# Kernel tuning notes

Hardware: AMD Instinct MI355X
Metric: run time of the kernel (lower is better)

## Reference

```python
import jax, jax.numpy as jnp
import numpy as np

DIM = 1024
NUM_HEADS = 16
HEAD_DIM = DIM // NUM_HEADS
SCALE = HEAD_DIM ** (-0.5)


def setup_inputs() -> dict:
    key = jax.random.key(0)
    ks = jax.random.split(key, 5)
    B, L, D = 2, 2048, DIM
    x = jax.random.normal(ks[0], (B, L, D), dtype=jnp.float32)
    # torch nn.Linear init scale ~ U(-1/sqrt(fan_in), 1/sqrt(fan_in)); use small normals
    s = 1.0 / np.sqrt(D)
    qkv_w = jax.random.uniform(ks[1], (3 * D, D), minval=-s, maxval=s, dtype=jnp.float32)
    qkv_b = jax.random.uniform(ks[2], (3 * D,), minval=-s, maxval=s, dtype=jnp.float32)
    proj_w = jax.random.uniform(ks[3], (D, D), minval=-s, maxval=s, dtype=jnp.float32)
    proj_b = jax.random.uniform(ks[4], (D,), minval=-s, maxval=s, dtype=jnp.float32)
    return {"x": x, "qkv_w": qkv_w, "qkv_b": qkv_b, "proj_w": proj_w, "proj_b": proj_b}


def reference(x, qkv_w, qkv_b, proj_w, proj_b):
    B, L, D = x.shape
    H, Hd = NUM_HEADS, HEAD_DIM
    # QKV projection: [B,L,3D] -> [3,B,H,L,Hd]
    qkv = x @ qkv_w.T + qkv_b
    qkv = qkv.reshape(B, L, 3, H, Hd).transpose(2, 0, 3, 1, 4)
    q, k, v = qkv[0], qkv[1], qkv[2]
    scores = jnp.einsum('bhqd,bhkd->bhqk', q, k) * SCALE  # [B,H,L,L]
    attn = jax.nn.softmax(scores, axis=-1)
    out = jnp.einsum('bhqk,bhkd->bhqd', attn, v)  # [B,H,L,Hd]
    out = out.transpose(0, 2, 1, 3).reshape(B, L, D)
    out = out @ proj_w.T + proj_b
    return out
```

## Files before the change

kernel.cpp:

```cpp
#include <hip/hip_runtime.h>
#include <hip/hip_bf16.h>
#include <cstdint>
#include <cstddef>

#define D_MODEL 1024
#define NHEADS 16
#define HD 64
#define NB 2
#define SL 2048
#define SEQ (NB*SL)
#define NQKV (3*D_MODEL)

typedef __attribute__((ext_vector_type(8))) short short8;
typedef __attribute__((ext_vector_type(4))) float floatx4;
typedef __attribute__((ext_vector_type(16))) float f32x16;
typedef unsigned short u16;

__device__ __forceinline__ u16 f2bf(float f) {
    union { float f; uint32_t u; } v; v.f = f;
    return (u16)((v.u + 0x7fffu + ((v.u >> 16) & 1u)) >> 16);
}

__device__ __forceinline__ uint32_t cvt_pk_bf16(float lo, float hi) {
    uint32_t r;
    asm("v_cvt_pk_bf16_f32 %0, %1, %2" : "=v"(r) : "v"(lo), "v"(hi));
    return r;
}

__device__ __forceinline__ void pl32swap(uint32_t &a, uint32_t &b) {
    asm("v_permlane32_swap_b32 %0, %1" : "+v"(a), "+v"(b));
}

__device__ __forceinline__ float exp2f_fast(float x) {
    float r; asm("v_exp_f32 %0, %1" : "=v"(r) : "v"(x)); return r;
}

__device__ __forceinline__ float m3f(float a, float b, float c) {
    return fmaxf(fmaxf(a, b), c);
}

__device__ __forceinline__ float vmax16(const f32x16& v) {
    float a0 = m3f(v[0], v[1], v[2]);
    float a1 = m3f(v[3], v[4], v[5]);
    float a2 = m3f(v[6], v[7], v[8]);
    float a3 = m3f(v[9], v[10], v[11]);
    float a4 = m3f(v[12], v[13], v[14]);
    return fmaxf(m3f(a0, a1, v[15]), m3f(a2, a3, a4));
}

__device__ __forceinline__ f32x16 zero16() {
    f32x16 z;
    #pragma unroll
    for (int i = 0; i < 16; i++) z[i] = 0.f;
    return z;
}

#define GLDS(gsrc, ldst) __builtin_amdgcn_global_load_lds( \
    (const __attribute__((address_space(1))) void*)(gsrc), \
    (__attribute__((address_space(3))) void*)(ldst), 16, 0, 0)

__global__ __launch_bounds__(256) void cvt_all(const float* __restrict__ x,
                                               const float* __restrict__ w1,
                                               const float* __restrict__ w2,
                                               u16* __restrict__ xb,
                                               u16* __restrict__ w1b,
                                               u16* __restrict__ w2b) {
    int i = blockIdx.x * 256 + threadIdx.x;
    const float4* src; ushort4* dst; int j;
    if (i < 1048576)      { src = (const float4*)x;  dst = (ushort4*)xb;  j = i; }
    else if (i < 1835008) { src = (const float4*)w1; dst = (ushort4*)w1b; j = i - 1048576; }
    else                  { src = (const float4*)w2; dst = (ushort4*)w2b; j = i - 1835008; }
    float4 f = src[j];
    ushort4 o;
    o.x = f2bf(f.x); o.y = f2bf(f.y); o.z = f2bf(f.z); o.w = f2bf(f.w);
    dst[j] = o;
}

__device__ __forceinline__ void gemm128_dbuf(const u16* __restrict__ A,
                                             const u16* __restrict__ B,
                                             int mbase, int nbase, int K,
                                             u16* Alds, u16* Blds,
                                             floatx4 acc[4][4]) {
    const int tid = threadIdx.x;
    const int lane = tid & 63;
    const int l15 = lane & 15, quad = lane >> 4;
    const int wave = tid >> 6;
    const int wr = wave >> 1, wc = wave & 1;
    #pragma unroll
    for (int i = 0; i < 4; i++)
        #pragma unroll
        for (int j = 0; j < 4; j++)
            acc[i][j] = (floatx4){0.f, 0.f, 0.f, 0.f};

    const int r0 = tid >> 2, kg0 = (tid & 3) * 8;
    const u16* Arow0 = A + (size_t)(mbase + r0) * K + kg0;
    const u16* Arow1 = A + (size_t)(mbase + r0 + 64) * K + kg0;
    const u16* Brow0 = B + (size_t)(nbase + r0) * K + kg0;
    const u16* Brow1 = B + (size_t)(nbase + r0 + 64) * K + kg0;

    GLDS(Arow0, Alds + tid * 8);
    GLDS(Arow1, Alds + (256 + tid) * 8);
    GLDS(Brow0, Blds + tid * 8);
    GLDS(Brow1, Blds + (256 + tid) * 8);
    __syncthreads();

    const int NT = K >> 5;
    for (int t = 0; t < NT; t++) {
        const int cur = t & 1;
        if (t + 1 < NT) {
            const int k0 = (t + 1) << 5;
            u16* Ad = Alds + (cur ^ 1) * 4096;
            u16* Bd = Blds + (cur ^ 1) * 4096;
            GLDS(Arow0 + k0, Ad + tid * 8);
            GLDS(Arow1 + k0, Ad + (256 + tid) * 8);
            GLDS(Brow0 + k0, Bd + tid * 8);
            GLDS(Brow1 + k0, Bd + (256 + tid) * 8);
        }
        const u16* Ac = Alds + cur * 4096;
        const u16* Bc = Blds + cur * 4096;
        short8 af[4], bf[4];
        #pragma unroll
        for (int i = 0; i < 4; i++)
            af[i] = *(const short8*)(Ac + (wr * 64 + i * 16 + l15) * 32 + quad * 8);
        #pragma unroll
        for (int j = 0; j < 4; j++)
            bf[j] = *(const short8*)(Bc + (wc * 64 + j * 16 + l15) * 32 + quad * 8);
        #pragma unroll
        for (int i = 0; i < 4; i++)
            #pragma unroll
            for (int j = 0; j < 4; j++)
                acc[i][j] = __builtin_amdgcn_mfma_f32_16x16x32_bf16(af[i], bf[j], acc[i][j], 0, 0, 0);
        __syncthreads();
    }
}

__global__ __launch_bounds__(256) void qkv_gemm(const u16* __restrict__ xb,
                                                const u16* __restrict__ wb,
                                                const float* __restrict__ bias,
                                                u16* __restrict__ Qo, u16* __restrict__ Ko,
                                                u16* __restrict__ Vt) {
    __shared__ __align__(16) u16 Alds[2 * 128 * 32];
    __shared__ __align__(16) u16 Blds[2 * 128 * 32];
    const int mbase = blockIdx.y * 128;
    const int nbase = blockIdx.x * 128;
    floatx4 acc[4][4];
    gemm128_dbuf(xb, wb, mbase, nbase, 1024, Alds, Blds, acc);
    const int lane = threadIdx.x & 63;
    const int wave = threadIdx.x >> 6;
    const int wr = wave >> 1, wc = wave & 1;
    const int l15 = lane & 15, quad = lane >> 4;
    const int which = nbase >> 10;
    #pragma unroll
    for (int j = 0; j < 4; j++) {
        int n = nbase + wc * 64 + j * 16 + l15;
        float bv = bias[n];
        int within = n & 1023;
        int h = within >> 6, d = within & 63;
        #pragma unroll
        for (int i = 0; i < 4; i++) {
            int m0 = mbase + wr * 64 + i * 16 + quad * 4;
            int b = m0 >> 11;
            int bh = b * NHEADS + h;
            if (which == 2) {
                int l0 = m0 & 2047;
                int slot = ((l0 >> 5) & 1) * 256 + ((l0 >> 4) & 1) * 128 + (d >> 5) * 64 + ((l0 >> 3) & 1) * 32 + (d & 31);
                ushort4 pk;
                pk.x = f2bf(acc[i][j][0] + bv); pk.y = f2bf(acc[i][j][1] + bv);
                pk.z = f2bf(acc[i][j][2] + bv); pk.w = f2bf(acc[i][j][3] + bv);
                *(ushort4*)(Vt + (size_t)bh * (SL * HD) + (size_t)(l0 >> 6) * 4096 + slot * 8 + (l0 & 7)) = pk;
            } else {
                #pragma unroll
                for (int r = 0; r < 4; r++) {
                    int m = m0 + r;
                    int l = m & 2047;
                    float v = acc[i][j][r] + bv;
                    if (which == 0) {
                        Qo[((size_t)bh * SL + l) * HD + d] = f2bf(v * 0.18033688f);
                    } else {
                        int slot = ((l >> 5) & 1) * 256 + (d >> 4) * 64 + ((d >> 3) & 1) * 32 + (l & 31);
                        Ko[(size_t)bh * (SL * HD) + (size_t)(l >> 6) * 4096 + slot * 8 + (d & 7)] = f2bf(v);
                    }
                }
            }
        }
    }
}

__global__ __launch_bounds__(512, 4) void flash_kernel(const u16* __restrict__ Q,
                                                       const u16* __restrict__ K,
                                                       const u16* __restrict__ V,
                                                       u16* __restrict__ AO) {
    __shared__ __align__(16) u16 smem[32768];
    const int tid = threadIdx.x;
    const int lane = tid & 63;
    const int wave = tid >> 6;
    const int qc = wave & 3;
    const int kvh = wave >> 2;
    const int tl = tid & 255;
    const int hi = lane >> 5;
    const int l31 = lane & 31;
    const int lane8 = lane * 8;

    const int bid = (int)blockIdx.x;
    const int swz = (bid & 7) * 64 + (bid >> 3);
    const int bh = swz >> 4;
    const int qb = swz & 15;
    const int b = bh >> 4, hd = bh & 15;
    const int qbase = qb * 128 + qc * 32;

    const u16* Qp = Q + (size_t)bh * SL * HD;
    const u16* Kg = K + (size_t)bh * (SL * HD) + (size_t)kvh * 16 * 4096;
    const u16* Vg = V + (size_t)bh * (SL * HD) + (size_t)kvh * 16 * 4096;

    u16* Kb_ = smem + kvh * 16384;
    u16* Vb_ = smem + kvh * 16384 + 8192;

    short8 qf[4];
    #pragma unroll
    for (int c = 0; c < 4; c++)
        qf[c] = *(const short8*)(Qp + (size_t)(qbase + l31) * HD + c * 16 + hi * 8);

    f32x16 accO0 = zero16(), accO1 = zero16();
    float m_i = -__builtin_inff();
    float l_i = 0.f;

    GLDS(Kg + tl * 8,         Kb_ + tl * 8);
    GLDS(Kg + (256 + tl) * 8, Kb_ + (256 + tl) * 8);
    GLDS(Vg + tl * 8,         Vb_ + tl * 8);
    GLDS(Vg + (256 + tl) * 8, Vb_ + (256 + tl) * 8);
    __syncthreads();

    union PW { uint32_t w[4]; short8 s8; };

    #pragma unroll 1
    for (int t = 0; t < 16; t++) {
        const int cur = t & 1;
        if (t + 1 < 16) {
            const u16* ks = Kg + (size_t)(t + 1) * 4096;
            const u16* vs = Vg + (size_t)(t + 1) * 4096;
            u16* kd = Kb_ + (cur ^ 1) * 4096;
            u16* vd = Vb_ + (cur ^ 1) * 4096;
            GLDS(ks + tl * 8,         kd + tl * 8);
            GLDS(ks + (256 + tl) * 8, kd + (256 + tl) * 8);
            GLDS(vs + tl * 8,         vd + tl * 8);
            GLDS(vs + (256 + tl) * 8, vd + (256 + tl) * 8);
        }
        const u16* Kt  = Kb_ + cur * 4096;
        const u16* Vt_ = Vb_ + cur * 4096;

        f32x16 sA = zero16(), sB = zero16();
        __builtin_amdgcn_s_setprio(1);
        #pragma unroll
        for (int c = 0; c < 4; c++) {
            short8 kf = *(const short8*)(Kt + c * 512 + lane8);
            sA = __builtin_amdgcn_mfma_f32_32x32x16_bf16(kf, qf[c], sA, 0, 0, 0);
        }
        #pragma unroll
        for (int c = 0; c < 4; c++) {
            short8 kf = *(const short8*)(Kt + 2048 + c * 512 + lane8);
            sB = __builtin_amdgcn_mfma_f32_32x32x16_bf16(kf, qf[c], sB, 0, 0, 0);
        }
        __builtin_amdgcn_s_setprio(0);

        float pmax = fmaxf(vmax16(sA), vmax16(sB));
        if (!__all(pmax - m_i <= 24.0f)) {
            float mo = m_i;
            float mn = fmaxf(mo, fmaxf(pmax, __shfl_xor(pmax, 32, 64)));
            m_i = mn;
            float alpha = exp2f_fast(mo - mn);
            l_i *= alpha;
            #pragma unroll
            for (int e = 0; e < 16; e++) { accO0[e] *= alpha; accO1[e] *= alpha; }
        }
        #pragma unroll
        for (int e = 0; e < 16; e++) sA[e] = exp2f_fast(sA[e] - m_i);
        #pragma unroll
        for (int e = 0; e < 16; e++) sB[e] = exp2f_fast(sB[e] - m_i);
        float r0 = 0.f, r1 = 0.f, r2 = 0.f, r3 = 0.f;
        #pragma unroll
        for (int e = 0; e < 16; e += 4) {
            r0 += sA[e]; r1 += sA[e + 1]; r2 += sA[e + 2]; r3 += sA[e + 3];
        }
        #pragma unroll
        for (int e = 0; e < 16; e += 4) {
            r0 += sB[e]; r1 += sB[e + 1]; r2 += sB[e + 2]; r3 += sB[e + 3];
        }
        float rs = (r0 + r1) + (r2 + r3);
        rs += __shfl_xor(rs, 32, 64);
        l_i += rs;

#define PV_SUB(SV, OFF) { \
        uint32_t a0 = cvt_pk_bf16(SV[0], SV[1]);  uint32_t b0 = cvt_pk_bf16(SV[4], SV[5]);  pl32swap(a0, b0); \
        uint32_t a1 = cvt_pk_bf16(SV[2], SV[3]);  uint32_t b1 = cvt_pk_bf16(SV[6], SV[7]);  pl32swap(a1, b1); \
        PW f0; f0.w[0] = a0; f0.w[1] = a1; f0.w[2] = b0; f0.w[3] = b1; \
        accO0 = __builtin_amdgcn_mfma_f32_32x32x16_bf16(*(const short8*)(Vt_ + (OFF) + lane8),        f0.s8, accO0, 0, 0, 0); \
        accO1 = __builtin_amdgcn_mfma_f32_32x32x16_bf16(*(const short8*)(Vt_ + (OFF) + 512 + lane8),  f0.s8, accO1, 0, 0, 0); \
        uint32_t c0 = cvt_pk_bf16(SV[8], SV[9]);  uint32_t d0 = cvt_pk_bf16(SV[12], SV[13]); pl32swap(c0, d0); \
        uint32_t c1 = cvt_pk_bf16(SV[10], SV[11]); uint32_t d1 = cvt_pk_bf16(SV[14], SV[15]); pl32swap(c1, d1); \
        PW f1; f1.w[0] = c0; f1.w[1] = c1; f1.w[2] = d0; f1.w[3] = d1; \
        accO0 = __builtin_amdgcn_mfma_f32_32x32x16_bf16(*(const short8*)(Vt_ + (OFF) + 1024 + lane8),       f1.s8, accO0, 0, 0, 0); \
        accO1 = __builtin_amdgcn_mfma_f32_32x32x16_bf16(*(const short8*)(Vt_ + (OFF) + 1024 + 512 + lane8), f1.s8, accO1, 0, 0, 0); }

        __builtin_amdgcn_s_setprio(1);
        PV_SUB(sA, 0);
        PV_SUB(sB, 2048);
        __builtin_amdgcn_s_setprio(0);
#undef PV_SUB

        __syncthreads();
    }

    float* xch = (float*)smem;
    if (kvh) {
        float* p = xch + (qc * 64 + lane) * 35;
        #pragma unroll
        for (int e = 0; e < 16; e++) { p[e] = accO0[e]; p[16 + e] = accO1[e]; }
        p[32] = m_i; p[33] = l_i;
    }
    __syncthreads();
    if (!kvh) {
        const float* p = xch + (qc * 64 + lane) * 35;
        float mB = p[32], lB = p[33];
        float m = fmaxf(m_i, mB);
        float s0 = exp2f_fast(m_i - m);
        float s1 = exp2f_fast(mB - m);
        float inv = 1.f / (s0 * l_i + s1 * lB);
        const size_t rowbase = ((size_t)(b * SL + qbase + l31)) * D_MODEL + hd * HD;
        #pragma unroll
        for (int rg = 0; rg < 4; rg++) {
            ushort4 o0, o1;
            o0.x = f2bf((s0 * accO0[rg * 4 + 0] + s1 * p[rg * 4 + 0]) * inv);
            o0.y = f2bf((s0 * accO0[rg * 4 + 1] + s1 * p[rg * 4 + 1]) * inv);
            o0.z = f2bf((s0 * accO0[rg * 4 + 2] + s1 * p[rg * 4 + 2]) * inv);
            o0.w = f2bf((s0 * accO0[rg * 4 + 3] + s1 * p[rg * 4 + 3]) * inv);
            *(ushort4*)(AO + rowbase + rg * 8 + 4 * hi) = o0;
            o1.x = f2bf((s0 * accO1[rg * 4 + 0] + s1 * p[16 + rg * 4 + 0]) * inv);
            o1.y = f2bf((s0 * accO1[rg * 4 + 1] + s1 * p[16 + rg * 4 + 1]) * inv);
            o1.z = f2bf((s0 * accO1[rg * 4 + 2] + s1 * p[16 + rg * 4 + 2]) * inv);
            o1.w = f2bf((s0 * accO1[rg * 4 + 3] + s1 * p[16 + rg * 4 + 3]) * inv);
            *(ushort4*)(AO + rowbase + 32 + rg * 8 + 4 * hi) = o1;
        }
    }
}

__global__ __launch_bounds__(256) void proj_gemm(const u16* __restrict__ ab,
                                                 const u16* __restrict__ wb,
                                                 const float* __restrict__ bias,
                                                 float* __restrict__ out) {
    __shared__ __align__(16) u16 Alds[2 * 128 * 32];
    __shared__ __align__(16) u16 Blds[2 * 128 * 32];
    const int mbase = blockIdx.y * 128;
    const int nbase = blockIdx.x * 128;
    floatx4 acc[4][4];
    gemm128_dbuf(ab, wb, mbase, nbase, 1024, Alds, Blds, acc);
    const int lane = threadIdx.x & 63;
    const int wave = threadIdx.x >> 6;
    const int wr = wave >> 1, wc = wave & 1;
    const int l15 = lane & 15, quad = lane >> 4;
    #pragma unroll
    for (int j = 0; j < 4; j++) {
        int n = nbase + wc * 64 + j * 16 + l15;
        float bv = bias[n];
        #pragma unroll
        for (int i = 0; i < 4; i++) {
            #pragma unroll
            for (int r = 0; r < 4; r++) {
                int m = mbase + wr * 64 + i * 16 + quad * 4 + r;
                out[(size_t)m * D_MODEL + n] = acc[i][j][r] + bv;
            }
        }
    }
}

extern "C" void kernel_launch(void* const* d_in, const int* in_sizes, int n_in,
                              void* d_out, int out_size, void* d_ws, size_t ws_size,
                              hipStream_t stream) {
    const float* x      = (const float*)d_in[0];
    const float* qkv_w  = (const float*)d_in[1];
    const float* qkv_b  = (const float*)d_in[2];
    const float* proj_w = (const float*)d_in[3];
    const float* proj_b = (const float*)d_in[4];
    float* out = (float*)d_out;
    char* ws = (char*)d_ws;

    u16* xb    = (u16*)(ws);
    u16* wqkv  = (u16*)(ws + 8388608);
    u16* wproj = (u16*)(ws + 14680064);
    u16* Qb    = (u16*)(ws + 16777216);
    u16* Kb    = (u16*)(ws + 25165824);
    u16* Vt    = (u16*)(ws + 33554432);
    u16* AO    = (u16*)(ws + 41943040);

    cvt_all<<<8192, 256, 0, stream>>>(x, qkv_w, proj_w, xb, wqkv, wproj);
    qkv_gemm<<<dim3(NQKV / 128, SEQ / 128), 256, 0, stream>>>(xb, wqkv, qkv_b, Qb, Kb, Vt);
    flash_kernel<<<dim3(512), 512, 0, stream>>>(Qb, Kb, Vt, AO);
    proj_gemm<<<dim3(D_MODEL / 128, SEQ / 128), 256, 0, stream>>>(AO, wproj, proj_b, out);
}
```

Baseline: 196.8 us.

## Use triple-buffered LDS pipeline with one barrier per K-step in GEMMs

Replaces the double-buffered GEMM main loop with a three-stage LDS ring. Loads are issued two tiles ahead, and a partial vmcnt wait plus a single barrier per iteration replaces the trailing __syncthreads. This is meant to hide more global-load latency and cut one barrier per step, at the cost of 50% more LDS per block, which may lower occupancy. The attention output buffer is also moved to reuse the xb workspace region, which is dead by then, to shrink the workspace footprint and possibly improve cache locality.

Result: no change. 197.2 us (+0.2%).

```diff
diff --git a/kernel.cpp b/kernel.cpp
--- a/kernel.cpp
+++ b/kernel.cpp
@@ -76,11 +76,11 @@
     dst[j] = o;
 }
 
-__device__ __forceinline__ void gemm128_dbuf(const u16* __restrict__ A,
-                                             const u16* __restrict__ B,
-                                             int mbase, int nbase, int K,
-                                             u16* Alds, u16* Blds,
-                                             floatx4 acc[4][4]) {
+__device__ __forceinline__ void gemm128_tri(const u16* __restrict__ A,
+                                            const u16* __restrict__ B,
+                                            int mbase, int nbase, int K,
+                                            u16* Alds, u16* Blds,
+                                            floatx4 acc[4][4]) {
     const int tid = threadIdx.x;
     const int lane = tid & 63;
     const int l15 = lane & 15, quad = lane >> 4;
@@ -98,26 +98,18 @@
     const u16* Brow0 = B + (size_t)(nbase + r0) * K + kg0;
     const u16* Brow1 = B + (size_t)(nbase + r0 + 64) * K + kg0;
 
-    GLDS(Arow0, Alds + tid * 8);
-    GLDS(Arow1, Alds + (256 + tid) * 8);
-    GLDS(Brow0, Blds + tid * 8);
-    GLDS(Brow1, Blds + (256 + tid) * 8);
-    __syncthreads();
-
-    const int NT = K >> 5;
-    for (int t = 0; t < NT; t++) {
-        const int cur = t & 1;
-        if (t + 1 < NT) {
-            const int k0 = (t + 1) << 5;
-            u16* Ad = Alds + (cur ^ 1) * 4096;
-            u16* Bd = Blds + (cur ^ 1) * 4096;
-            GLDS(Arow0 + k0, Ad + tid * 8);
-            GLDS(Arow1 + k0, Ad + (256 + tid) * 8);
-            GLDS(Brow0 + k0, Bd + tid * 8);
-            GLDS(Brow1 + k0, Bd + (256 + tid) * 8);
-        }
-        const u16* Ac = Alds + cur * 4096;
-        const u16* Bc = Blds + cur * 4096;
+    auto stage = [&](int t, int buf) {
+        const int k0 = t << 5;
+        u16* Ad = Alds + buf * 4096;
+        u16* Bd = Blds + buf * 4096;
+        GLDS(Arow0 + k0, Ad + tid * 8);
+        GLDS(Arow1 + k0, Ad + (256 + tid) * 8);
+        GLDS(Brow0 + k0, Bd + tid * 8);
+        GLDS(Brow1 + k0, Bd + (256 + tid) * 8);
+    };
+    auto compute = [&](int buf) {
+        const u16* Ac = Alds + buf * 4096;
+        const u16* Bc = Blds + buf * 4096;
         short8 af[4], bf[4];
         #pragma unroll
         for (int i = 0; i < 4; i++)
@@ -130,8 +122,23 @@
             #pragma unroll
             for (int j = 0; j < 4; j++)
                 acc[i][j] = __builtin_amdgcn_mfma_f32_16x16x32_bf16(af[i], bf[j], acc[i][j], 0, 0, 0);
-        __syncthreads();
-    }
+    };
+
+    const int NT = K >> 5;
+    stage(0, 0);
+    stage(1, 1);
+    int c0 = 0, c2 = 2;
+    for (int t = 0; t < NT - 1; ++t) {
+        asm volatile("s_waitcnt vmcnt(4)" ::: "memory");
+        __builtin_amdgcn_s_barrier();
+        if (t + 2 < NT) stage(t + 2, c2);
+        compute(c0);
+        c0 = (c0 == 2) ? 0 : c0 + 1;
+        c2 = (c2 == 2) ? 0 : c2 + 1;
+    }
+    asm volatile("s_waitcnt vmcnt(0)" ::: "memory");
+    __builtin_amdgcn_s_barrier();
+    compute(c0);
 }
 
 __global__ __launch_bounds__(256) void qkv_gemm(const u16* __restrict__ xb,
@@ -139,12 +146,12 @@
                                                 const float* __restrict__ bias,
                                                 u16* __restrict__ Qo, u16* __restrict__ Ko,
                                                 u16* __restrict__ Vt) {
-    __shared__ __align__(16) u16 Alds[2 * 128 * 32];
-    __shared__ __align__(16) u16 Blds[2 * 128 * 32];
+    __shared__ __align__(16) u16 Alds[3 * 128 * 32];
+    __shared__ __align__(16) u16 Blds[3 * 128 * 32];
     const int mbase = blockIdx.y * 128;
     const int nbase = blockIdx.x * 128;
     floatx4 acc[4][4];
-    gemm128_dbuf(xb, wb, mbase, nbase, 1024, Alds, Blds, acc);
+    gemm128_tri(xb, wb, mbase, nbase, 1024, Alds, Blds, acc);
     const int lane = threadIdx.x & 63;
     const int wave = threadIdx.x >> 6;
     const int wr = wave >> 1, wc = wave & 1;
@@ -347,12 +354,12 @@
                                                  const u16* __restrict__ wb,
                                                  const float* __restrict__ bias,
                                                  float* __restrict__ out) {
-    __shared__ __align__(16) u16 Alds[2 * 128 * 32];
-    __shared__ __align__(16) u16 Blds[2 * 128 * 32];
+    __shared__ __align__(16) u16 Alds[3 * 128 * 32];
+    __shared__ __align__(16) u16 Blds[3 * 128 * 32];
     const int mbase = blockIdx.y * 128;
     const int nbase = blockIdx.x * 128;
     floatx4 acc[4][4];
-    gemm128_dbuf(ab, wb, mbase, nbase, 1024, Alds, Blds, acc);
+    gemm128_tri(ab, wb, mbase, nbase, 1024, Alds, Blds, acc);
     const int lane = threadIdx.x & 63;
     const int wave = threadIdx.x >> 6;
     const int wr = wave >> 1, wc = wave & 1;
@@ -389,7 +396,7 @@
     u16* Qb    = (u16*)(ws + 16777216);
     u16* Kb    = (u16*)(ws + 25165824);
     u16* Vt    = (u16*)(ws + 33554432);
-    u16* AO    = (u16*)(ws + 41943040);
+    u16* AO    = (u16*)(ws);
 
     cvt_all<<<8192, 256, 0, stream>>>(x, qkv_w, proj_w, xb, wqkv, wproj);
     qkv_gemm<<<dim3(NQKV / 128, SEQ / 128), 256, 0, stream>>>(xb, wqkv, qkv_b, Qb, Kb, Vt);
```

## Use BK=64 fragment-ordered LDS layout in GEMMs with MFMA priority boost

Applied to the files above, without the earlier changes.

The shared GEMM helper moves from a K-tile of 32 to a K-tile of 64. The LDS layout is rearranged into MFMA fragment order, so each lane reads contiguous 16-byte chunks and avoids bank-conflicted strided reads. It also raises wave priority around the MFMA block with s_setprio. The attention-output buffer now reuses the start of the workspace (the bf16 x buffer, which is dead by then), shrinking the footprint. The larger tile halves the number of barriers and loop iterations, at the cost of twice the LDS per block (64KB), which may reduce occupancy.

Measured after the change: 220.8 us. +12.2%, slower.

```diff
diff --git a/kernel.cpp b/kernel.cpp
--- a/kernel.cpp
+++ b/kernel.cpp
@@ -76,14 +76,13 @@
     dst[j] = o;
 }
 
-__device__ __forceinline__ void gemm128_dbuf(const u16* __restrict__ A,
+__device__ __forceinline__ void gemm128_bk64(const u16* __restrict__ A,
                                              const u16* __restrict__ B,
-                                             int mbase, int nbase, int K,
+                                             int mbase, int nbase,
                                              u16* Alds, u16* Blds,
                                              floatx4 acc[4][4]) {
     const int tid = threadIdx.x;
     const int lane = tid & 63;
-    const int l15 = lane & 15, quad = lane >> 4;
     const int wave = tid >> 6;
     const int wr = wave >> 1, wc = wave & 1;
     #pragma unroll
@@ -92,44 +91,60 @@
         for (int j = 0; j < 4; j++)
             acc[i][j] = (floatx4){0.f, 0.f, 0.f, 0.f};
 
-    const int r0 = tid >> 2, kg0 = (tid & 3) * 8;
-    const u16* Arow0 = A + (size_t)(mbase + r0) * K + kg0;
-    const u16* Arow1 = A + (size_t)(mbase + r0 + 64) * K + kg0;
-    const u16* Brow0 = B + (size_t)(nbase + r0) * K + kg0;
-    const u16* Brow1 = B + (size_t)(nbase + r0 + 64) * K + kg0;
-
-    GLDS(Arow0, Alds + tid * 8);
-    GLDS(Arow1, Alds + (256 + tid) * 8);
-    GLDS(Brow0, Blds + tid * 8);
-    GLDS(Brow1, Blds + (256 + tid) * 8);
+    const u16* srcA[4]; const u16* srcB[4]; int dOff[4];
+    #pragma unroll
+    for (int r = 0; r < 4; r++) {
+        int s = r * 256 + tid;
+        int ls = s & 15, qs = (s >> 4) & 3, kk = (s >> 6) & 1, fi = (s >> 7) & 3, hf = s >> 9;
+        int row = hf * 64 + fi * 16 + ls;
+        int col = kk * 32 + qs * 8;
+        srcA[r] = A + (size_t)(mbase + row) * 1024 + col;
+        srcB[r] = B + (size_t)(nbase + row) * 1024 + col;
+        dOff[r] = s * 8;
+    }
+    const int rdA = wr * 4096 + lane * 8;
+    const int rdB = wc * 4096 + lane * 8;
+
+    #pragma unroll
+    for (int r = 0; r < 4; r++) GLDS(srcA[r], Alds + dOff[r]);
+    #pragma unroll
+    for (int r = 0; r < 4; r++) GLDS(srcB[r], Blds + dOff[r]);
     __syncthreads();
 
-    const int NT = K >> 5;
-    for (int t = 0; t < NT; t++) {
+    #pragma unroll 1
+    for (int t = 0; t < 16; t++) {
         const int cur = t & 1;
-        if (t + 1 < NT) {
-            const int k0 = (t + 1) << 5;
-            u16* Ad = Alds + (cur ^ 1) * 4096;
-            u16* Bd = Blds + (cur ^ 1) * 4096;
-            GLDS(Arow0 + k0, Ad + tid * 8);
-            GLDS(Arow1 + k0, Ad + (256 + tid) * 8);
-            GLDS(Brow0 + k0, Bd + tid * 8);
-            GLDS(Brow1 + k0, Bd + (256 + tid) * 8);
-        }
-        const u16* Ac = Alds + cur * 4096;
-        const u16* Bc = Blds + cur * 4096;
-        short8 af[4], bf[4];
+        if (t < 15) {
+            const int kc = (t + 1) * 64;
+            u16* Ad = Alds + (cur ^ 1) * 8192;
+            u16* Bd = Blds + (cur ^ 1) * 8192;
+            #pragma unroll
+            for (int r = 0; r < 4; r++) GLDS(srcA[r] + kc, Ad + dOff[r]);
+            #pragma unroll
+            for (int r = 0; r < 4; r++) GLDS(srcB[r] + kc, Bd + dOff[r]);
+        }
+        const u16* Ac = Alds + cur * 8192;
+        const u16* Bc = Blds + cur * 8192;
+        short8 af[4][2], bf[4][2];
         #pragma unroll
         for (int i = 0; i < 4; i++)
-            af[i] = *(const short8*)(Ac + (wr * 64 + i * 16 + l15) * 32 + quad * 8);
+            #pragma unroll
+            for (int kk = 0; kk < 2; kk++)
+                af[i][kk] = *(const short8*)(Ac + rdA + (i * 2 + kk) * 512);
         #pragma unroll
         for (int j = 0; j < 4; j++)
-            bf[j] = *(const short8*)(Bc + (wc * 64 + j * 16 + l15) * 32 + quad * 8);
+            #pragma unroll
+            for (int kk = 0; kk < 2; kk++)
+                bf[j][kk] = *(const short8*)(Bc + rdB + (j * 2 + kk) * 512);
+        __builtin_amdgcn_s_setprio(1);
         #pragma unroll
         for (int i = 0; i < 4; i++)
             #pragma unroll
             for (int j = 0; j < 4; j++)
-                acc[i][j] = __builtin_amdgcn_mfma_f32_16x16x32_bf16(af[i], bf[j], acc[i][j], 0, 0, 0);
+                #pragma unroll
+                for (int kk = 0; kk < 2; kk++)
+                    acc[i][j] = __builtin_amdgcn_mfma_f32_16x16x32_bf16(af[i][kk], bf[j][kk], acc[i][j], 0, 0, 0);
+        __builtin_amdgcn_s_setprio(0);
         __syncthreads();
     }
 }
@@ -139,12 +154,12 @@
                                                 const float* __restrict__ bias,
                                                 u16* __restrict__ Qo, u16* __restrict__ Ko,
                                                 u16* __restrict__ Vt) {
-    __shared__ __align__(16) u16 Alds[2 * 128 * 32];
-    __shared__ __align__(16) u16 Blds[2 * 128 * 32];
+    __shared__ __align__(16) u16 Alds[2 * 8192];
+    __shared__ __align__(16) u16 Blds[2 * 8192];
     const int mbase = blockIdx.y * 128;
     const int nbase = blockIdx.x * 128;
     floatx4 acc[4][4];
-    gemm128_dbuf(xb, wb, mbase, nbase, 1024, Alds, Blds, acc);
+    gemm128_bk64(xb, wb, mbase, nbase, Alds, Blds, acc);
     const int lane = threadIdx.x & 63;
     const int wave = threadIdx.x >> 6;
     const int wr = wave >> 1, wc = wave & 1;
@@ -347,12 +362,12 @@
                                                  const u16* __restrict__ wb,
                                                  const float* __restrict__ bias,
                                                  float* __restrict__ out) {
-    __shared__ __align__(16) u16 Alds[2 * 128 * 32];
-    __shared__ __align__(16) u16 Blds[2 * 128 * 32];
+    __shared__ __align__(16) u16 Alds[2 * 8192];
+    __shared__ __align__(16) u16 Blds[2 * 8192];
     const int mbase = blockIdx.y * 128;
     const int nbase = blockIdx.x * 128;
     floatx4 acc[4][4];
-    gemm128_dbuf(ab, wb, mbase, nbase, 1024, Alds, Blds, acc);
+    gemm128_bk64(ab, wb, mbase, nbase, Alds, Blds, acc);
     const int lane = threadIdx.x & 63;
     const int wave = threadIdx.x >> 6;
     const int wr = wave >> 1, wc = wave & 1;
@@ -389,7 +404,7 @@
     u16* Qb    = (u16*)(ws + 16777216);
     u16* Kb    = (u16*)(ws + 25165824);
     u16* Vt    = (u16*)(ws + 33554432);
-    u16* AO    = (u16*)(ws + 41943040);
+    u16* AO    = (u16*)(ws);
 
     cvt_all<<<8192, 256, 0, stream>>>(x, qkv_w, proj_w, xb, wqkv, wproj);
     qkv_gemm<<<dim3(NQKV / 128, SEQ / 128), 256, 0, stream>>>(xb, wqkv, qkv_b, Qb, Kb, Vt);
```
